# Kernel optimization log

Hardware: AMD Instinct MI355X
Metric: run time of the kernel (lower is better)

The kernel has to match this reference:

```python
import jax, jax.numpy as jnp
import numpy as np

# OmniNet(deepqmc) reconstruction: ElectronicSchNet v1 (2 interactions, kernel_dim=8,
# embedding_dim=16, dist_feat_dim=4) + Linear(16,1,bias=False) orbital + sum over electrons.
# SchNet v1: shared w and g per interaction, spin-dependent h (same/anti), nuclear
# messages via learned nuclear embeddings Y. Subnets: w = 2-layer log-DNN 4->6->8 with SSP,
# h = Linear(16,8), g = Linear(8,16). SSP(x) = softplus(x) - log(2).

N_UP, N_DOWN = 16, 16
N_ELEC = N_UP + N_DOWN
N_ATOMS = 8
DIST_FEAT, KERNEL, EMBED = 4, 8, 16
N_INTER = 2
BATCH = 4096


def ssp(x):
    return jax.nn.softplus(x) - jnp.log(2.0).astype(x.dtype)


def setup_inputs() -> dict:
    key = jax.random.key(0)
    ks = jax.random.split(key, 16)
    s = 0.5  # init scale
    return {
        'dists_nuc': jax.random.uniform(ks[0], (BATCH, N_ELEC, N_ATOMS, DIST_FEAT), jnp.float32),
        'dists_elec': jax.random.uniform(ks[1], (BATCH, N_ELEC, N_ELEC, DIST_FEAT), jnp.float32),
        'X': jax.random.normal(ks[2], (1, EMBED), jnp.float32) * s,          # electron embedding (n_up==n_down)
        'Y': jax.random.normal(ks[3], (N_ATOMS, KERNEL), jnp.float32) * s,   # nuclear embeddings
        'w1': jax.random.normal(ks[4], (N_INTER, DIST_FEAT, 6), jnp.float32) * s,
        'wb1': jax.random.normal(ks[5], (N_INTER, 6), jnp.float32) * s,
        'w2': jax.random.normal(ks[6], (N_INTER, 6, KERNEL), jnp.float32) * s,
        'wb2': jax.random.normal(ks[7], (N_INTER, KERNEL), jnp.float32) * s,
        'hs_w': jax.random.normal(ks[8], (N_INTER, EMBED, KERNEL), jnp.float32) * s,
        'hs_b': jax.random.normal(ks[9], (N_INTER, KERNEL), jnp.float32) * s,
        'ha_w': jax.random.normal(ks[10], (N_INTER, EMBED, KERNEL), jnp.float32) * s,
        'ha_b': jax.random.normal(ks[11], (N_INTER, KERNEL), jnp.float32) * s,
        'g_w': jax.random.normal(ks[12], (N_INTER, KERNEL, EMBED), jnp.float32) * s,
        'g_b': jax.random.normal(ks[13], (N_INTER, EMBED), jnp.float32) * s,
        'orb_w': jax.random.normal(ks[14], (EMBED,), jnp.float32) * s,
    }


def reference(dists_nuc, dists_elec, X, Y, w1, wb1, w2, wb2, hs_w, hs_b, ha_w, ha_b, g_w, g_b, orb_w):
    B, n_elec = dists_elec.shape[:2]
    dt = dists_elec.dtype
    spins = jnp.concatenate([jnp.zeros(N_UP, jnp.int32), jnp.ones(N_DOWN, jnp.int32)])
    eye = jnp.eye(n_elec, dtype=bool)
    same = ((spins[:, None] == spins[None, :]) & ~eye).astype(dt)  # (i,j) same-spin, no self
    anti = (spins[:, None] != spins[None, :]).astype(dt)

    # initial embeddings: all electrons share X[0] since n_up == n_down
    x = jnp.broadcast_to(X[0], (B, n_elec, EMBED))

    for n in range(N_INTER):
        def w_net(e):  # (..., 4) -> (..., 8)
            return ssp(e @ w1[n] + wb1[n]) @ w2[n] + wb2[n]
        we = w_net(dists_elec)            # (B, i, j, K)
        wn = w_net(dists_nuc)             # (B, i, M, K)
        hs = x @ hs_w[n] + hs_b[n]        # (B, j, K) same-spin message features
        ha = x @ ha_w[n] + ha_b[n]        # (B, j, K) anti-spin
        z = (jnp.einsum('bijk,ij,bjk->bik', we, same, hs)
             + jnp.einsum('bijk,ij,bjk->bik', we, anti, ha)
             + jnp.einsum('bimk,mk->bik', wn, Y))
        x = x + (z @ g_w[n] + g_b[n])     # residual update

    # orbital projection (Linear(16,1,bias=False)), squeeze, sum over electrons
    return (x @ orb_w).sum(axis=-1)       # (B,)
```

## Files before the change

### kernel.cpp

```cpp
#include <hip/hip_runtime.h>

#define NE 32
#define NA 8
#define DF 4
#define KD 8
#define ED 16
#define BATCH 4096

#define WS_W1S0 0
#define WS_W1S1 24
#define WS_B1S0 48
#define WS_B1S1 54
#define WS_B2H0 60
#define WS_B2H1 68
#define WS_MS0  76
#define WS_MA0  84
#define WS_MS   92
#define WS_MA   156
#define WS_CS   220
#define WS_CA   228
#define WS_GO0  236
#define WS_GO1  244
#define WS_BASE 252

typedef float f32x2 __attribute__((ext_vector_type(2)));
__device__ __forceinline__ f32x2 splat2(float s) { f32x2 r; r.x = s; r.y = s; return r; }
__device__ __forceinline__ f32x2 fma2(f32x2 a, f32x2 b, f32x2 c) {
    return __builtin_elementwise_fma(a, b, c);
}

__global__ void omni_setup(const float* __restrict__ X,   const float* __restrict__ w1,
                           const float* __restrict__ wb1, const float* __restrict__ w2,
                           const float* __restrict__ wb2, const float* __restrict__ hs_w,
                           const float* __restrict__ hs_b,const float* __restrict__ ha_w,
                           const float* __restrict__ ha_b,const float* __restrict__ g_w,
                           const float* __restrict__ g_b, const float* __restrict__ orb_w,
                           float* __restrict__ ws)
{
    const int t = threadIdx.x;
    const float L   = 1.4426950408889634f;
    const float LN2 = 0.6931471805599453f;
    if (t < 48) {
        ws[t] = w1[t] * L;
    } else if (t < 60) {
        ws[t] = wb1[t - 48] * L;
    } else if (t < 76) {
        const int u = t - 60, n = u >> 3, k = u & 7;
        float sw = 0.f;
        for (int a = 0; a < 6; ++a) sw += w2[n * 48 + a * KD + k];
        ws[t] = wb2[n * KD + k] * L - sw;
    } else if (t < 92) {
        const int u = t - 76, tab = u >> 3, k = u & 7;
        const float* mw = tab ? ha_w : hs_w;
        const float* mb = tab ? ha_b : hs_b;
        float acc = mb[k];
        for (int c = 0; c < ED; ++c) acc += X[c] * mw[c * KD + k];
        ws[t] = acc;
    } else if (t < 220) {
        int u = t - 92; const int tab = u >> 6; u &= 63;
        const int kp = u >> 3, k = u & 7;
        const float* mw = (tab ? ha_w : hs_w) + ED * KD;
        float acc = 0.f;
        for (int c = 0; c < ED; ++c)
            acc += LN2 * g_w[kp * ED + c] * mw[c * KD + k];
        ws[t] = acc;
    } else if (t < 236) {
        const int u = t - 220, tab = u >> 3, k = u & 7;
        const float* mw = (tab ? ha_w : hs_w) + ED * KD;
        const float* mb = (tab ? ha_b : hs_b) + KD;
        float acc = mb[k];
        for (int c = 0; c < ED; ++c) acc += (X[c] + g_b[c]) * mw[c * KD + k];
        ws[t] = acc;
    } else if (t < 252) {
        const int u = t - 236, n = u >> 3, k = u & 7;
        float acc = 0.f;
        for (int c = 0; c < ED; ++c)
            acc += LN2 * g_w[n * KD * ED + k * ED + c] * orb_w[c];
        ws[t] = acc;
    } else if (t == 252) {
        float acc = 0.f;
        for (int c = 0; c < ED; ++c) acc += (X[c] + g_b[c] + g_b[ED + c]) * orb_w[c];
        ws[t] = acc;
    }
}

__device__ __forceinline__ void wnet_r2(const float4 e,
                                        const f32x2* __restrict__ vB1s2,
                                        const f32x2* __restrict__ sW12,
                                        f32x2* __restrict__ r2)
{
    #pragma unroll
    for (int a2 = 0; a2 < 3; ++a2) {
        f32x2 u = fma2(splat2(e.x), sW12[a2], vB1s2[a2]);
        u = fma2(splat2(e.y), sW12[3 + a2], u);
        u = fma2(splat2(e.z), sW12[6 + a2], u);
        u = fma2(splat2(e.w), sW12[9 + a2], u);
        f32x2 t;
        t.x = __builtin_amdgcn_exp2f(u.x);
        t.y = __builtin_amdgcn_exp2f(u.y);
        t = t + splat2(1.0f);
        r2[a2].x = __builtin_amdgcn_logf(t.x);
        r2[a2].y = __builtin_amdgcn_logf(t.y);
    }
}

__device__ __forceinline__ void proj2(const f32x2* __restrict__ r2,
                                      const f32x2* __restrict__ sW22,
                                      const f32x2* __restrict__ vB2h2,
                                      f32x2* __restrict__ racc2)
{
    #pragma unroll
    for (int k2 = 0; k2 < 4; ++k2) {
        f32x2 acc = vB2h2[k2];
        acc = fma2(splat2(r2[0].x), sW22[0 * 4 + k2], acc);
        acc = fma2(splat2(r2[0].y), sW22[1 * 4 + k2], acc);
        acc = fma2(splat2(r2[1].x), sW22[2 * 4 + k2], acc);
        acc = fma2(splat2(r2[1].y), sW22[3 * 4 + k2], acc);
        acc = fma2(splat2(r2[2].x), sW22[4 * 4 + k2], acc);
        acc = fma2(splat2(r2[2].y), sW22[5 * 4 + k2], acc);
        racc2[k2] = acc;
    }
}

__global__ __launch_bounds__(128)
__attribute__((amdgpu_waves_per_eu(4, 4)))
void omni_main(
    const float* __restrict__ dists_nuc,
    const float* __restrict__ dists_elec,
    const float* __restrict__ Y,
    const float* __restrict__ w2,
    const float* __restrict__ ws,
    float* __restrict__ out)
{
    const int tid  = threadIdx.x;
    const int h    = tid >> 6;
    const int lane = tid & 63;
    const int il   = lane & 15;
    const int jh   = lane >> 4;
    const int ig   = 16 * h + il;
    const int b    = blockIdx.x;
    const int sj   = jh >> 1;
    const bool same = (sj == h);
    const int t32  = same ? 0 : 32;

    __shared__ float msg[65][KD];
    __shared__ float part[2];
    if (tid < KD) msg[64][tid] = 0.0f;

    const f32x2* ws2  = (const f32x2*)ws;
    const f32x2* w2p0 = (const f32x2*)w2;
    const f32x2* w2p1 = (const f32x2*)(w2 + 48);
    const f32x2* Yp   = (const f32x2*)Y;

    const float* de = dists_elec + (((size_t)b * NE + ig) * NE + 8 * jh) * DF;
    const float* dn = dists_nuc  + (((size_t)b * NE + ig) * NA + 2 * jh) * DF;

    float4 er[8];
    float4 nr[2];
    #pragma unroll
    for (int s = 0; s < 8; ++s) er[s] = ((const float4*)de)[s];
    nr[0] = ((const float4*)dn)[0];
    nr[1] = ((const float4*)dn)[1];

    float zr0[KD];
    {
        f32x2 vB1s2[3], vB2h2[4], msel2[4];
        #pragma unroll
        for (int a2 = 0; a2 < 3; ++a2) vB1s2[a2] = ws2[WS_B1S0 / 2 + a2];
        #pragma unroll
        for (int k2 = 0; k2 < 4; ++k2) vB2h2[k2] = ws2[WS_B2H0 / 2 + k2];
        #pragma unroll
        for (int k2 = 0; k2 < 4; ++k2)
            msel2[k2] = same ? ws2[WS_MS0 / 2 + k2] : ws2[WS_MA0 / 2 + k2];

        const int scnt  = ig - 8 * jh;
        const float fcnt = (jh == (ig >> 3)) ? 7.0f : 8.0f;
        f32x2 S2[3] = {splat2(0.f), splat2(0.f), splat2(0.f)};
        #pragma unroll
        for (int s = 0; s < 8; ++s) {
            f32x2 r2[3];
            wnet_r2(er[s], vB1s2, ws2 + WS_W1S0 / 2, r2);
            const float mf = (s == scnt) ? 0.0f : 1.0f;
            #pragma unroll
            for (int a2 = 0; a2 < 3; ++a2) S2[a2] = fma2(r2[a2], splat2(mf), S2[a2]);
        }
        f32x2 z2[4];
        #pragma unroll
        for (int k2 = 0; k2 < 4; ++k2) {
            f32x2 acc = splat2(fcnt) * vB2h2[k2];
            acc = fma2(splat2(S2[0].x), w2p0[0 * 4 + k2], acc);
            acc = fma2(splat2(S2[0].y), w2p0[1 * 4 + k2], acc);
            acc = fma2(splat2(S2[1].x), w2p0[2 * 4 + k2], acc);
            acc = fma2(splat2(S2[1].y), w2p0[3 * 4 + k2], acc);
            acc = fma2(splat2(S2[2].x), w2p0[4 * 4 + k2], acc);
            acc = fma2(splat2(S2[2].y), w2p0[5 * 4 + k2], acc);
            z2[k2] = acc * msel2[k2];
        }
        {
            f32x2 r2[3], racc2[4];
            wnet_r2(nr[0], vB1s2, ws2 + WS_W1S0 / 2, r2);
            proj2(r2, w2p0, vB2h2, racc2);
            #pragma unroll
            for (int k2 = 0; k2 < 4; ++k2)
                z2[k2] = fma2(racc2[k2], Yp[(2 * jh) * 4 + k2], z2[k2]);
            wnet_r2(nr[1], vB1s2, ws2 + WS_W1S0 / 2, r2);
            proj2(r2, w2p0, vB2h2, racc2);
            #pragma unroll
            for (int k2 = 0; k2 < 4; ++k2)
                z2[k2] = fma2(racc2[k2], Yp[(2 * jh + 1) * 4 + k2], z2[k2]);
        }
        #pragma unroll
        for (int k2 = 0; k2 < 4; ++k2) {
            float za = z2[k2].x, zb = z2[k2].y;
            za += __shfl_xor(za, 16, 64); za += __shfl_xor(za, 32, 64);
            zb += __shfl_xor(zb, 16, 64); zb += __shfl_xor(zb, 32, 64);
            zr0[2 * k2] = za; zr0[2 * k2 + 1] = zb;
        }
    }

    {
        f32x2 ms2[4], ma2[4];
        #pragma unroll
        for (int k2 = 0; k2 < 4; ++k2) {
            ms2[k2] = ws2[WS_CS / 2 + k2];
            ma2[k2] = ws2[WS_CA / 2 + k2];
        }
        #pragma unroll
        for (int kp = 0; kp < KD; ++kp) {
            const f32x2 zk = splat2(zr0[kp]);
            #pragma unroll
            for (int k2 = 0; k2 < 4; ++k2) {
                ms2[k2] = fma2(zk, ws2[WS_MS / 2 + kp * 4 + k2], ms2[k2]);
                ma2[k2] = fma2(zk, ws2[WS_MA / 2 + kp * 4 + k2], ma2[k2]);
            }
        }
        if (jh == 0) {
            #pragma unroll
            for (int k2 = 0; k2 < 4; ++k2) *(f32x2*)&msg[ig][2 * k2] = ms2[k2];
        } else if (jh == 2) {
            #pragma unroll
            for (int k2 = 0; k2 < 4; ++k2) *(f32x2*)&msg[32 + ig][2 * k2] = ma2[k2];
        }
    }

    float dot = ws[WS_BASE];
    #pragma unroll
    for (int k = 0; k < KD; ++k) dot = fmaf(zr0[k], ws[WS_GO0 + k], dot);

    __syncthreads();

    float zr1[KD];
    {
        f32x2 vB1s2[3], vB2h2[4];
        #pragma unroll
        for (int a2 = 0; a2 < 3; ++a2) vB1s2[a2] = ws2[WS_B1S1 / 2 + a2];
        #pragma unroll
        for (int k2 = 0; k2 < 4; ++k2) vB2h2[k2] = ws2[WS_B2H1 / 2 + k2];

        f32x2 z2[4] = {splat2(0.f), splat2(0.f), splat2(0.f), splat2(0.f)};
        #pragma unroll
        for (int s = 0; s < 8; ++s) {
            f32x2 r2[3], racc2[4];
            wnet_r2(er[s], vB1s2, ws2 + WS_W1S1 / 2, r2);
            proj2(r2, w2p1, vB2h2, racc2);
            const int j = 8 * jh + s;
            const int row = (j == ig) ? 64 : (t32 + j);
            const f32x2* mrow = (const f32x2*)&msg[row][0];
            #pragma unroll
            for (int k2 = 0; k2 < 4; ++k2) z2[k2] = fma2(racc2[k2], mrow[k2], z2[k2]);
        }
        {
            f32x2 r2[3], racc2[4];
            wnet_r2(nr[0], vB1s2, ws2 + WS_W1S1 / 2, r2);
            proj2(r2, w2p1, vB2h2, racc2);
            #pragma unroll
            for (int k2 = 0; k2 < 4; ++k2)
                z2[k2] = fma2(racc2[k2], Yp[(2 * jh) * 4 + k2], z2[k2]);
            wnet_r2(nr[1], vB1s2, ws2 + WS_W1S1 / 2, r2);
            proj2(r2, w2p1, vB2h2, racc2);
            #pragma unroll
            for (int k2 = 0; k2 < 4; ++k2)
                z2[k2] = fma2(racc2[k2], Yp[(2 * jh + 1) * 4 + k2], z2[k2]);
        }
        #pragma unroll
        for (int k2 = 0; k2 < 4; ++k2) {
            float za = z2[k2].x, zb = z2[k2].y;
            za += __shfl_xor(za, 16, 64); za += __shfl_xor(za, 32, 64);
            zb += __shfl_xor(zb, 16, 64); zb += __shfl_xor(zb, 32, 64);
            zr1[2 * k2] = za; zr1[2 * k2 + 1] = zb;
        }
    }

    #pragma unroll
    for (int k = 0; k < KD; ++k) dot = fmaf(zr1[k], ws[WS_GO1 + k], dot);
    dot *= 0.25f;
    #pragma unroll
    for (int off = 1; off < 64; off <<= 1) dot += __shfl_xor(dot, off, 64);
    if (lane == 0) part[h] = dot;
    __syncthreads();
    if (tid == 0) out[b] = part[0] + part[1];
}

extern "C" void kernel_launch(void* const* d_in, const int* in_sizes, int n_in,
                              void* d_out, int out_size, void* d_ws, size_t ws_size,
                              hipStream_t stream) {
    const float* dists_nuc  = (const float*)d_in[0];
    const float* dists_elec = (const float*)d_in[1];
    const float* X     = (const float*)d_in[2];
    const float* Y     = (const float*)d_in[3];
    const float* w1    = (const float*)d_in[4];
    const float* wb1   = (const float*)d_in[5];
    const float* w2    = (const float*)d_in[6];
    const float* wb2   = (const float*)d_in[7];
    const float* hs_w  = (const float*)d_in[8];
    const float* hs_b  = (const float*)d_in[9];
    const float* ha_w  = (const float*)d_in[10];
    const float* ha_b  = (const float*)d_in[11];
    const float* g_w   = (const float*)d_in[12];
    const float* g_b   = (const float*)d_in[13];
    const float* orb_w = (const float*)d_in[14];
    float* out = (float*)d_out;
    float* ws  = (float*)d_ws;

    omni_setup<<<1, 256, 0, stream>>>(X, w1, wb1, w2, wb2, hs_w, hs_b,
                                      ha_w, ha_b, g_w, g_b, orb_w, ws);
    omni_main<<<BATCH, 128, 0, stream>>>(dists_nuc, dists_elec, Y, w2, ws, out);
}
```

Before: 146.1 us.

## Precompute interaction-1 filter outputs before the barrier to overlap with sync

The second interaction's w-net filter values for all electron and nuclear pairs are now computed in the first phase, before the __syncthreads, and held in an 80-register array. After the barrier only the message-weighted accumulation is left, so the filter math can overlap with the first phase instead of sitting on the critical path after the sync. The occupancy hint is relaxed to allow 3 waves per EU to make room for the extra registers. This risks lower occupancy or spills.

```diff
diff --git a/kernel.cpp b/kernel.cpp
--- a/kernel.cpp
+++ b/kernel.cpp
@@ -123,7 +123,7 @@
 }
 
 __global__ __launch_bounds__(128)
-__attribute__((amdgpu_waves_per_eu(4, 4)))
+__attribute__((amdgpu_waves_per_eu(3, 4)))
 void omni_main(
     const float* __restrict__ dists_nuc,
     const float* __restrict__ dists_elec,
@@ -162,32 +162,40 @@
     nr[0] = ((const float4*)dn)[0];
     nr[1] = ((const float4*)dn)[1];
 
+    f32x2 racc1[40];
+
     float zr0[KD];
     {
-        f32x2 vB1s2[3], vB2h2[4], msel2[4];
-        #pragma unroll
-        for (int a2 = 0; a2 < 3; ++a2) vB1s2[a2] = ws2[WS_B1S0 / 2 + a2];
-        #pragma unroll
-        for (int k2 = 0; k2 < 4; ++k2) vB2h2[k2] = ws2[WS_B2H0 / 2 + k2];
-        #pragma unroll
-        for (int k2 = 0; k2 < 4; ++k2)
+        f32x2 vB1s0[3], vB1s1[3], vB2h0[4], vB2h1[4], msel2[4];
+        #pragma unroll
+        for (int a2 = 0; a2 < 3; ++a2) {
+            vB1s0[a2] = ws2[WS_B1S0 / 2 + a2];
+            vB1s1[a2] = ws2[WS_B1S1 / 2 + a2];
+        }
+        #pragma unroll
+        for (int k2 = 0; k2 < 4; ++k2) {
+            vB2h0[k2] = ws2[WS_B2H0 / 2 + k2];
+            vB2h1[k2] = ws2[WS_B2H1 / 2 + k2];
             msel2[k2] = same ? ws2[WS_MS0 / 2 + k2] : ws2[WS_MA0 / 2 + k2];
+        }
 
         const int scnt  = ig - 8 * jh;
         const float fcnt = (jh == (ig >> 3)) ? 7.0f : 8.0f;
         f32x2 S2[3] = {splat2(0.f), splat2(0.f), splat2(0.f)};
         #pragma unroll
         for (int s = 0; s < 8; ++s) {
-            f32x2 r2[3];
-            wnet_r2(er[s], vB1s2, ws2 + WS_W1S0 / 2, r2);
+            f32x2 r0[3], r1[3];
+            wnet_r2(er[s], vB1s0, ws2 + WS_W1S0 / 2, r0);
+            wnet_r2(er[s], vB1s1, ws2 + WS_W1S1 / 2, r1);
             const float mf = (s == scnt) ? 0.0f : 1.0f;
             #pragma unroll
-            for (int a2 = 0; a2 < 3; ++a2) S2[a2] = fma2(r2[a2], splat2(mf), S2[a2]);
+            for (int a2 = 0; a2 < 3; ++a2) S2[a2] = fma2(r0[a2], splat2(mf), S2[a2]);
+            proj2(r1, w2p1, vB2h1, &racc1[s * 4]);
         }
         f32x2 z2[4];
         #pragma unroll
         for (int k2 = 0; k2 < 4; ++k2) {
-            f32x2 acc = splat2(fcnt) * vB2h2[k2];
+            f32x2 acc = splat2(fcnt) * vB2h0[k2];
             acc = fma2(splat2(S2[0].x), w2p0[0 * 4 + k2], acc);
             acc = fma2(splat2(S2[0].y), w2p0[1 * 4 + k2], acc);
             acc = fma2(splat2(S2[1].x), w2p0[2 * 4 + k2], acc);
@@ -196,18 +204,16 @@
             acc = fma2(splat2(S2[2].y), w2p0[5 * 4 + k2], acc);
             z2[k2] = acc * msel2[k2];
         }
-        {
-            f32x2 r2[3], racc2[4];
-            wnet_r2(nr[0], vB1s2, ws2 + WS_W1S0 / 2, r2);
-            proj2(r2, w2p0, vB2h2, racc2);
+        #pragma unroll
+        for (int t = 0; t < 2; ++t) {
+            f32x2 r0[3], r1[3], racc0[4];
+            wnet_r2(nr[t], vB1s0, ws2 + WS_W1S0 / 2, r0);
+            wnet_r2(nr[t], vB1s1, ws2 + WS_W1S1 / 2, r1);
+            proj2(r0, w2p0, vB2h0, racc0);
+            proj2(r1, w2p1, vB2h1, &racc1[(8 + t) * 4]);
             #pragma unroll
             for (int k2 = 0; k2 < 4; ++k2)
-                z2[k2] = fma2(racc2[k2], Yp[(2 * jh) * 4 + k2], z2[k2]);
-            wnet_r2(nr[1], vB1s2, ws2 + WS_W1S0 / 2, r2);
-            proj2(r2, w2p0, vB2h2, racc2);
-            #pragma unroll
-            for (int k2 = 0; k2 < 4; ++k2)
-                z2[k2] = fma2(racc2[k2], Yp[(2 * jh + 1) * 4 + k2], z2[k2]);
+                z2[k2] = fma2(racc0[k2], Yp[(2 * jh + t) * 4 + k2], z2[k2]);
         }
         #pragma unroll
         for (int k2 = 0; k2 < 4; ++k2) {
@@ -251,36 +257,21 @@
 
     float zr1[KD];
     {
-        f32x2 vB1s2[3], vB2h2[4];
-        #pragma unroll
-        for (int a2 = 0; a2 < 3; ++a2) vB1s2[a2] = ws2[WS_B1S1 / 2 + a2];
-        #pragma unroll
-        for (int k2 = 0; k2 < 4; ++k2) vB2h2[k2] = ws2[WS_B2H1 / 2 + k2];
-
         f32x2 z2[4] = {splat2(0.f), splat2(0.f), splat2(0.f), splat2(0.f)};
         #pragma unroll
         for (int s = 0; s < 8; ++s) {
-            f32x2 r2[3], racc2[4];
-            wnet_r2(er[s], vB1s2, ws2 + WS_W1S1 / 2, r2);
-            proj2(r2, w2p1, vB2h2, racc2);
             const int j = 8 * jh + s;
             const int row = (j == ig) ? 64 : (t32 + j);
             const f32x2* mrow = (const f32x2*)&msg[row][0];
             #pragma unroll
-            for (int k2 = 0; k2 < 4; ++k2) z2[k2] = fma2(racc2[k2], mrow[k2], z2[k2]);
-        }
-        {
-            f32x2 r2[3], racc2[4];
-            wnet_r2(nr[0], vB1s2, ws2 + WS_W1S1 / 2, r2);
-            proj2(r2, w2p1, vB2h2, racc2);
-            #pragma unroll
             for (int k2 = 0; k2 < 4; ++k2)
-                z2[k2] = fma2(racc2[k2], Yp[(2 * jh) * 4 + k2], z2[k2]);
-            wnet_r2(nr[1], vB1s2, ws2 + WS_W1S1 / 2, r2);
-            proj2(r2, w2p1, vB2h2, racc2);
+                z2[k2] = fma2(racc1[s * 4 + k2], mrow[k2], z2[k2]);
+        }
+        #pragma unroll
+        for (int t = 0; t < 2; ++t) {
             #pragma unroll
             for (int k2 = 0; k2 < 4; ++k2)
-                z2[k2] = fma2(racc2[k2], Yp[(2 * jh + 1) * 4 + k2], z2[k2]);
+                z2[k2] = fma2(racc1[(8 + t) * 4 + k2], Yp[(2 * jh + t) * 4 + k2], z2[k2]);
         }
         #pragma unroll
         for (int k2 = 0; k2 < 4; ++k2) {
```

Result: no change. 144.9 us (-0.8%).
